# Kernel tuning notes

Hardware: AMD Instinct MI355X
Metric: run time of the kernel (lower is better)

## Reference

```python
import jax, jax.numpy as jnp
import numpy as np

EPS = 1e-6
NUM_HEADS = 4


def setup_inputs() -> dict:
    key = jax.random.key(0)
    ks = jax.random.split(key, 7)
    B, C, H, W = 4, 128, 64, 64
    x = jax.random.normal(ks[0], (B, C, H, W), dtype=jnp.float32)
    norm_w = jnp.ones((C,), dtype=jnp.float32)
    norm_b = jnp.zeros((C,), dtype=jnp.float32)
    # 1x1 convs stored as [out_ch, in_ch] matrices
    qkv_w = jax.random.normal(ks[1], (3 * C, C), dtype=jnp.float32) / np.sqrt(C)
    qkv_b = jnp.zeros((3 * C,), dtype=jnp.float32)
    proj_w = jax.random.normal(ks[2], (C, C), dtype=jnp.float32) / np.sqrt(C)
    proj_b = jnp.zeros((C,), dtype=jnp.float32)
    return {"x": x, "norm_w": norm_w, "norm_b": norm_b,
            "qkv_w": qkv_w, "qkv_b": qkv_b, "proj_w": proj_w, "proj_b": proj_b}


def reference(x, norm_w, norm_b, qkv_w, qkv_b, proj_w, proj_b):
    B, C, H, W = x.shape
    nh = NUM_HEADS
    dh = C // nh
    N = H * W

    # ChannelLayerNorm: stats over channel dim per spatial position
    mean = jnp.mean(x, axis=1, keepdims=True)
    var = jnp.mean(jnp.square(x - mean), axis=1, keepdims=True)  # unbiased=False
    h = (x - mean) * jax.lax.rsqrt(var + EPS)
    h = h * norm_w[None, :, None, None] + norm_b[None, :, None, None]

    # qkv 1x1 conv -> [B, 3C, H, W]
    qkv = jnp.einsum('oc,bchw->bohw', qkv_w, h) + qkv_b[None, :, None, None]
    qkv = qkv.reshape(B, 3, nh, dh, N)
    q, k, v = qkv[:, 0], qkv[:, 1], qkv[:, 2]  # each [B, nh, dh, N]

    scale = dh ** -0.5
    attn = jnp.einsum('bhcn,bhcm->bhnm', q, k) * scale  # [B, nh, N, N]
    attn = jax.nn.softmax(attn, axis=-1)
    h = jnp.einsum('bhnm,bhcm->bhcn', attn, v)  # [B, nh, dh, N]
    h = h.reshape(B, C, H, W)

    h = jnp.einsum('oc,bchw->bohw', proj_w, h) + proj_b[None, :, None, None]
    return x + h
```

## Files before the change

### kernel.cpp

```cpp
#include <hip/hip_runtime.h>
#include <hip/hip_bf16.h>
#include <math.h>

#define BB 4
#define CC 128
#define NH 4
#define DH 32
#define NN 4096
#define OC3 (3*CC)

typedef __attribute__((ext_vector_type(8))) short short8;
typedef __attribute__((ext_vector_type(4))) short short4v;
typedef __attribute__((ext_vector_type(4))) float float4v;

__device__ inline short f2bf(float f) {
    unsigned u = __builtin_bit_cast(unsigned, f);
    u += 0x7FFF + ((u >> 16) & 1);
    return (short)(u >> 16);
}
__device__ inline unsigned pk2bf(float a, float b) {
    __hip_bfloat162 h = __float22bfloat162_rn(make_float2(a, b));
    unsigned u; __builtin_memcpy(&u, &h, 4);
    return u;
}

#define HS 136
__global__ __launch_bounds__(512, 4) void lnqkv_kernel(
        const float* __restrict__ x, const float* __restrict__ nw,
        const float* __restrict__ nb, const float* __restrict__ qw,
        const float* __restrict__ qbias,
        short* __restrict__ qT, short* __restrict__ kT, short* __restrict__ vv) {
    __shared__ short hT[64 * HS];
    __shared__ float red[16][64];
    __shared__ float mrs[2][64];
    int t = threadIdx.x;
    int n0g = blockIdx.x * 64;
    int b = n0g >> 12, n0 = n0g & (NN - 1);
    int nl = t & 63, cq = t >> 6;

    const float* xp = x + ((size_t)b * CC + cq * 16) * NN + n0 + nl;
    float xv[16];
    float s = 0.f, ss = 0.f;
    #pragma unroll
    for (int j = 0; j < 16; ++j) {
        xv[j] = xp[(size_t)j * NN];
        s += xv[j]; ss += xv[j] * xv[j];
    }
    red[cq][nl] = s; red[cq + 8][nl] = ss;
    __syncthreads();
    if (t < 64) {
        float s8 = 0.f, q8 = 0.f;
        #pragma unroll
        for (int j = 0; j < 8; ++j) { s8 += red[j][t]; q8 += red[j + 8][t]; }
        float mean = s8 * (1.0f / CC);
        float var  = q8 * (1.0f / CC) - mean * mean;
        mrs[0][t] = mean;
        mrs[1][t] = rsqrtf(var + 1e-6f);
    }
    __syncthreads();
    {
        float mean = mrs[0][nl], rsv = mrs[1][nl];
        #pragma unroll
        for (int j = 0; j < 16; j += 8) {
            union { short8 v; unsigned u[4]; } z;
            #pragma unroll
            for (int k = 0; k < 4; ++k) {
                int c = cq * 16 + j + 2 * k;
                float h0 = (xv[j + 2 * k]     - mean) * rsv * nw[c]     + nb[c];
                float h1 = (xv[j + 2 * k + 1] - mean) * rsv * nw[c + 1] + nb[c + 1];
                z.u[k] = pk2bf(h0, h1);
            }
            *(short8*)&hT[nl * HS + cq * 16 + j] = z.v;
        }
    }
    __syncthreads();

    int w = t >> 6, lane = t & 63;
    int lg = lane >> 4, ln = lane & 15;
    #pragma unroll
    for (int it = 0; it < 3; ++it) {
        int ow = (w + it * 8) * 16;
        const float* wp = qw + (size_t)(ow + ln) * CC;
        float4v a0 = {0,0,0,0}, a1 = {0,0,0,0}, a2 = {0,0,0,0}, a3 = {0,0,0,0};
        #pragma unroll
        for (int cs = 0; cs < 4; ++cs) {
            float4 wa = *(const float4*)(wp + cs * 32 + lg * 8);
            float4 wb = *(const float4*)(wp + cs * 32 + lg * 8 + 4);
            union { short8 v; unsigned u[4]; } af;
            af.u[0] = pk2bf(wa.x, wa.y); af.u[1] = pk2bf(wa.z, wa.w);
            af.u[2] = pk2bf(wb.x, wb.y); af.u[3] = pk2bf(wb.z, wb.w);
            const short* hp = &hT[cs * 32 + lg * 8];
            a0 = __builtin_amdgcn_mfma_f32_16x16x32_bf16(af.v, *(const short8*)&hp[(0  + ln) * HS], a0, 0, 0, 0);
            a1 = __builtin_amdgcn_mfma_f32_16x16x32_bf16(af.v, *(const short8*)&hp[(16 + ln) * HS], a1, 0, 0, 0);
            a2 = __builtin_amdgcn_mfma_f32_16x16x32_bf16(af.v, *(const short8*)&hp[(32 + ln) * HS], a2, 0, 0, 0);
            a3 = __builtin_amdgcn_mfma_f32_16x16x32_bf16(af.v, *(const short8*)&hp[(48 + ln) * HS], a3, 0, 0, 0);
        }
        int r0 = ow + lg * 4;
        float b0 = qbias[r0], b1 = qbias[r0 + 1], b2 = qbias[r0 + 2], b3 = qbias[r0 + 3];
        int cb = ow & 31;
        float4v* accs[4] = {&a0, &a1, &a2, &a3};
        if (it == 0) {
            const float qs = 0.1767766952966369f * 1.4426950408889634f;
            int hh = ow >> 5;
            size_t rowbase = (size_t)(b * NH + hh) * NN + n0;
            #pragma unroll
            for (int nsub = 0; nsub < 4; ++nsub) {
                float4v av = *accs[nsub];
                union { short4v v; unsigned u[2]; } z;
                z.u[0] = pk2bf((av.x + b0) * qs, (av.y + b1) * qs);
                z.u[1] = pk2bf((av.z + b2) * qs, (av.w + b3) * qs);
                *(short4v*)&qT[(rowbase + nsub * 16 + ln) * DH + cb + lg * 4] = z.v;
            }
        } else if (it == 1) {
            int hh = (ow - CC) >> 5;
            size_t rowbase = (size_t)(b * NH + hh) * NN + n0;
            #pragma unroll
            for (int nsub = 0; nsub < 4; ++nsub) {
                float4v av = *accs[nsub];
                union { short4v v; unsigned u[2]; } z;
                z.u[0] = pk2bf(av.x + b0, av.y + b1);
                z.u[1] = pk2bf(av.z + b2, av.w + b3);
                *(short4v*)&kT[(rowbase + nsub * 16 + ln) * DH + cb + lg * 4] = z.v;
            }
        } else {
            int hh = (ow - 2 * CC) >> 5;
            size_t cbase = (size_t)((b * NH + hh) * DH + cb + lg * 4);
            #pragma unroll
            for (int nsub = 0; nsub < 4; ++nsub) {
                float4v av = *accs[nsub];
                size_t col = (size_t)n0 + nsub * 16 + ln;
                vv[(cbase + 0) * NN + col] = f2bf(av.x + b0);
                vv[(cbase + 1) * NN + col] = f2bf(av.y + b1);
                vv[(cbase + 2) * NN + col] = f2bf(av.z + b2);
                vv[(cbase + 3) * NN + col] = f2bf(av.w + b3);
            }
        }
    }
}

#define PS 72
union __align__(16) FlashSh {
    short pt[8 * 16 * PS];
    struct { float mo[3][8][64][8]; float ml[3][8][64]; } m;
};
__global__ __launch_bounds__(512, 2) void flash_kernel(
        const short* __restrict__ qT, const short* __restrict__ kT,
        const short* __restrict__ vv, short* __restrict__ aoT) {
    __shared__ FlashSh sh;
    int blk = blockIdx.x;
    int bh = blk >> 5;
    int qb = blk & 31;
    int b = bh >> 2, hh = bh & 3;
    int n0 = qb * 128;
    int t = threadIdx.x, w = t >> 6, lane = t & 63;
    int lg = lane >> 4, ln = lane & 15;
    int qg = w & 1;
    int split = w >> 1;

    const short* kbase = kT + (size_t)bh * NN * DH + lg * 8;
    const short* vb0 = vv + ((size_t)bh * DH + ln) * NN + lg * 8;
    const short* vb1 = vb0 + (size_t)16 * NN;

    short8 qf[4];
    #pragma unroll
    for (int j = 0; j < 4; ++j)
        qf[j] = *(const short8*)&qT[((size_t)bh * NN + n0 + (qg * 4 + j) * 16 + ln) * DH + lg * 8];

    float4v o0[4], o1[4];
    float ls[4];
    #pragma unroll
    for (int j = 0; j < 4; ++j) {
        o0[j] = (float4v){0,0,0,0}; o1[j] = (float4v){0,0,0,0}; ls[j] = 0.f;
    }
    short* ptw = &sh.pt[w * 16 * PS];

    int mbeg = split * (NN / 4), mend = mbeg + NN / 4;
    for (int m0 = mbeg; m0 < mend; m0 += 64) {
        const short* kp = kbase + (size_t)m0 * DH;
        short8 k0 = *(const short8*)(kp + (size_t)(ln +  0) * DH);
        short8 k1 = *(const short8*)(kp + (size_t)(ln + 16) * DH);
        short8 k2 = *(const short8*)(kp + (size_t)(ln + 32) * DH);
        short8 k3 = *(const short8*)(kp + (size_t)(ln + 48) * DH);
        short8 v0 = *(const short8*)(vb0 + m0);
        short8 v1 = *(const short8*)(vb0 + m0 + 32);
        short8 v2 = *(const short8*)(vb1 + m0);
        short8 v3 = *(const short8*)(vb1 + m0 + 32);

        #pragma unroll
        for (int j = 0; j < 4; ++j) {
            float4v s0 = {0,0,0,0}, s1 = s0, s2 = s0, s3 = s0;
            s0 = __builtin_amdgcn_mfma_f32_16x16x32_bf16(k0, qf[j], s0, 0, 0, 0);
            s1 = __builtin_amdgcn_mfma_f32_16x16x32_bf16(k1, qf[j], s1, 0, 0, 0);
            s2 = __builtin_amdgcn_mfma_f32_16x16x32_bf16(k2, qf[j], s2, 0, 0, 0);
            s3 = __builtin_amdgcn_mfma_f32_16x16x32_bf16(k3, qf[j], s3, 0, 0, 0);
            float lacc = 0.f;
            float4v* sv[4] = {&s0, &s1, &s2, &s3};
            #pragma unroll
            for (int jj = 0; jj < 4; ++jj) {
                float4v sj = *sv[jj];
                float p0 = __builtin_amdgcn_exp2f(sj.x);
                float p1 = __builtin_amdgcn_exp2f(sj.y);
                float p2 = __builtin_amdgcn_exp2f(sj.z);
                float p3 = __builtin_amdgcn_exp2f(sj.w);
                lacc += (p0 + p1) + (p2 + p3);
                union { short4v v; unsigned u[2]; } z;
                z.u[0] = pk2bf(p0, p1); z.u[1] = pk2bf(p2, p3);
                *(short4v*)&ptw[ln * PS + jj * 16 + lg * 4] = z.v;
            }
            ls[j] += lacc;
            short8 pb0 = *(const short8*)&ptw[ln * PS + 0  + lg * 8];
            short8 pb1 = *(const short8*)&ptw[ln * PS + 32 + lg * 8];
            o0[j] = __builtin_amdgcn_mfma_f32_16x16x32_bf16(v0, pb0, o0[j], 0, 0, 0);
            o1[j] = __builtin_amdgcn_mfma_f32_16x16x32_bf16(v2, pb0, o1[j], 0, 0, 0);
            o0[j] = __builtin_amdgcn_mfma_f32_16x16x32_bf16(v1, pb1, o0[j], 0, 0, 0);
            o1[j] = __builtin_amdgcn_mfma_f32_16x16x32_bf16(v3, pb1, o1[j], 0, 0, 0);
        }
    }

    __syncthreads();
    if (split > 0) {
        int si = split - 1;
        #pragma unroll
        for (int j = 0; j < 4; ++j) {
            int tid = qg * 4 + j;
            float* mp = &sh.m.mo[si][tid][lane][0];
            *(float4*)(mp + 0) = make_float4(o0[j].x, o0[j].y, o0[j].z, o0[j].w);
            *(float4*)(mp + 4) = make_float4(o1[j].x, o1[j].y, o1[j].z, o1[j].w);
            sh.m.ml[si][tid][lane] = ls[j];
        }
    }
    __syncthreads();
    if (split == 0) {
        #pragma unroll
        for (int j = 0; j < 4; ++j) {
            int tid = qg * 4 + j;
            #pragma unroll
            for (int si = 0; si < 3; ++si) {
                const float* mp = &sh.m.mo[si][tid][lane][0];
                float4 a0 = *(const float4*)(mp + 0);
                float4 a1 = *(const float4*)(mp + 4);
                o0[j].x += a0.x; o0[j].y += a0.y; o0[j].z += a0.z; o0[j].w += a0.w;
                o1[j].x += a1.x; o1[j].y += a1.y; o1[j].z += a1.z; o1[j].w += a1.w;
                ls[j] += sh.m.ml[si][tid][lane];
            }
            float lt = ls[j];
            lt += __shfl_xor(lt, 16, 64);
            lt += __shfl_xor(lt, 32, 64);
            float inv = 1.0f / lt;
            short* ap = aoT + ((size_t)b * NN + n0 + tid * 16 + ln) * CC + hh * DH;
            union { short4v v; unsigned u[2]; } z;
            z.u[0] = pk2bf(o0[j].x * inv, o0[j].y * inv);
            z.u[1] = pk2bf(o0[j].z * inv, o0[j].w * inv);
            *(short4v*)&ap[lg * 4] = z.v;
            z.u[0] = pk2bf(o1[j].x * inv, o1[j].y * inv);
            z.u[1] = pk2bf(o1[j].z * inv, o1[j].w * inv);
            *(short4v*)&ap[16 + lg * 4] = z.v;
        }
    }
}

__global__ __launch_bounds__(256) void proj_kernel(
        const short* __restrict__ aoT, const float* __restrict__ pw,
        const float* __restrict__ pb, const float* __restrict__ x,
        float* __restrict__ out) {
    int t = threadIdx.x;
    int n0g = blockIdx.x * 64;
    int b = n0g >> 12, n0 = n0g & (NN - 1);
    int o0 = blockIdx.y * 64;
    int wo = t >> 6, lane = t & 63;
    int lg = lane >> 4, ln = lane & 15;
    int ow = o0 + wo * 16;
    const float* wp = pw + (size_t)(ow + ln) * CC;
    const short* ap = aoT + (size_t)n0g * CC + lg * 8;
    float4v a0 = {0,0,0,0}, a1 = {0,0,0,0}, a2 = {0,0,0,0}, a3 = {0,0,0,0};
    #pragma unroll
    for (int cs = 0; cs < 4; ++cs) {
        float4 wa = *(const float4*)(wp + cs * 32 + lg * 8);
        float4 wb = *(const float4*)(wp + cs * 32 + lg * 8 + 4);
        union { short8 v; unsigned u[4]; } af;
        af.u[0] = pk2bf(wa.x, wa.y); af.u[1] = pk2bf(wa.z, wa.w);
        af.u[2] = pk2bf(wb.x, wb.y); af.u[3] = pk2bf(wb.z, wb.w);
        const short* hp = ap + cs * 32;
        a0 = __builtin_amdgcn_mfma_f32_16x16x32_bf16(af.v, *(const short8*)&hp[(size_t)(0  + ln) * CC], a0, 0, 0, 0);
        a1 = __builtin_amdgcn_mfma_f32_16x16x32_bf16(af.v, *(const short8*)&hp[(size_t)(16 + ln) * CC], a1, 0, 0, 0);
        a2 = __builtin_amdgcn_mfma_f32_16x16x32_bf16(af.v, *(const short8*)&hp[(size_t)(32 + ln) * CC], a2, 0, 0, 0);
        a3 = __builtin_amdgcn_mfma_f32_16x16x32_bf16(af.v, *(const short8*)&hp[(size_t)(48 + ln) * CC], a3, 0, 0, 0);
    }
    int r0 = ow + lg * 4;
    float b0 = pb[r0], b1 = pb[r0 + 1], b2 = pb[r0 + 2], b3 = pb[r0 + 3];
    const float* xbase = x   + ((size_t)b * CC + r0) * NN + n0 + ln;
    float*       obase = out + ((size_t)b * CC + r0) * NN + n0 + ln;
    float4v* accs[4] = {&a0, &a1, &a2, &a3};
    #pragma unroll
    for (int nsub = 0; nsub < 4; ++nsub) {
        float4v av = *accs[nsub];
        const float* xp = xbase + nsub * 16;
        float* op = obase + nsub * 16;
        op[(size_t)0 * NN] = av.x + b0 + xp[(size_t)0 * NN];
        op[(size_t)1 * NN] = av.y + b1 + xp[(size_t)1 * NN];
        op[(size_t)2 * NN] = av.z + b2 + xp[(size_t)2 * NN];
        op[(size_t)3 * NN] = av.w + b3 + xp[(size_t)3 * NN];
    }
}

extern "C" void kernel_launch(void* const* d_in, const int* in_sizes, int n_in,
                              void* d_out, int out_size, void* d_ws, size_t ws_size,
                              hipStream_t stream) {
    const float* x    = (const float*)d_in[0];
    const float* nw   = (const float*)d_in[1];
    const float* nb   = (const float*)d_in[2];
    const float* qkvw = (const float*)d_in[3];
    const float* qkvb = (const float*)d_in[4];
    const float* pw   = (const float*)d_in[5];
    const float* pb   = (const float*)d_in[6];
    float* out = (float*)d_out;

    short* qT  = (short*)d_ws;
    short* kT  = qT + (size_t)BB * NH * NN * DH;
    short* vv  = kT + (size_t)BB * NH * NN * DH;
    short* aoT = vv + (size_t)BB * NH * DH * NN;

    lnqkv_kernel<<<dim3(256), 512, 0, stream>>>(x, nw, nb, qkvw, qkvb, qT, kT, vv);
    flash_kernel<<<dim3(512), 512, 0, stream>>>(qT, kT, vv, aoT);
    proj_kernel<<<dim3(256, 2), 256, 0, stream>>>(aoT, pw, pb, x, out);
}
```

Baseline: 145.7 us.

## Shrink flash blocks to 32 queries with 4 KV-split waves and tree merge

Each flash block now covers 32 queries with 256 threads: 4 waves, each handling a quarter of the keys, instead of 128 queries with 8 waves. The grid grows from 512 to 2048 blocks, and the cross-wave reduction becomes a two-level tree in shared memory. The aim is more blocks per CU and better load balance across the GPU. The cost is that each wave handles 2 query tiles instead of 4, so K/V loads are reused across fewer queries and global K/V traffic per query rises about twofold.

```diff
diff --git a/kernel.cpp b/kernel.cpp
--- a/kernel.cpp
+++ b/kernel.cpp
@@ -140,36 +140,35 @@
 
 #define PS 72
 union __align__(16) FlashSh {
-    short pt[8 * 16 * PS];
-    struct { float mo[3][8][64][8]; float ml[3][8][64]; } m;
+    short pt[4 * 16 * PS];
+    struct { float mo[2][2][64][8]; float ml[2][2][64]; } m;
 };
-__global__ __launch_bounds__(512, 2) void flash_kernel(
+__global__ __launch_bounds__(256, 8) void flash_kernel(
         const short* __restrict__ qT, const short* __restrict__ kT,
         const short* __restrict__ vv, short* __restrict__ aoT) {
     __shared__ FlashSh sh;
     int blk = blockIdx.x;
-    int bh = blk >> 5;
-    int qb = blk & 31;
+    int bh = blk >> 7;
+    int qb = blk & 127;
     int b = bh >> 2, hh = bh & 3;
-    int n0 = qb * 128;
+    int n0 = qb * 32;
     int t = threadIdx.x, w = t >> 6, lane = t & 63;
     int lg = lane >> 4, ln = lane & 15;
-    int qg = w & 1;
-    int split = w >> 1;
+    int split = w;
 
     const short* kbase = kT + (size_t)bh * NN * DH + lg * 8;
     const short* vb0 = vv + ((size_t)bh * DH + ln) * NN + lg * 8;
     const short* vb1 = vb0 + (size_t)16 * NN;
 
-    short8 qf[4];
-    #pragma unroll
-    for (int j = 0; j < 4; ++j)
-        qf[j] = *(const short8*)&qT[((size_t)bh * NN + n0 + (qg * 4 + j) * 16 + ln) * DH + lg * 8];
-
-    float4v o0[4], o1[4];
-    float ls[4];
-    #pragma unroll
-    for (int j = 0; j < 4; ++j) {
+    short8 qf[2];
+    #pragma unroll
+    for (int j = 0; j < 2; ++j)
+        qf[j] = *(const short8*)&qT[((size_t)bh * NN + n0 + j * 16 + ln) * DH + lg * 8];
+
+    float4v o0[2], o1[2];
+    float ls[2];
+    #pragma unroll
+    for (int j = 0; j < 2; ++j) {
         o0[j] = (float4v){0,0,0,0}; o1[j] = (float4v){0,0,0,0}; ls[j] = 0.f;
     }
     short* ptw = &sh.pt[w * 16 * PS];
@@ -187,7 +186,7 @@
         short8 v3 = *(const short8*)(vb1 + m0 + 32);
 
         #pragma unroll
-        for (int j = 0; j < 4; ++j) {
+        for (int j = 0; j < 2; ++j) {
             float4v s0 = {0,0,0,0}, s1 = s0, s2 = s0, s3 = s0;
             s0 = __builtin_amdgcn_mfma_f32_16x16x32_bf16(k0, qf[j], s0, 0, 0, 0);
             s1 = __builtin_amdgcn_mfma_f32_16x16x32_bf16(k1, qf[j], s1, 0, 0, 0);
@@ -218,36 +217,55 @@
     }
 
     __syncthreads();
-    if (split > 0) {
-        int si = split - 1;
-        #pragma unroll
-        for (int j = 0; j < 4; ++j) {
-            int tid = qg * 4 + j;
-            float* mp = &sh.m.mo[si][tid][lane][0];
+    if (split & 1) {
+        int slot = split >> 1;
+        #pragma unroll
+        for (int j = 0; j < 2; ++j) {
+            float* mp = &sh.m.mo[slot][j][lane][0];
             *(float4*)(mp + 0) = make_float4(o0[j].x, o0[j].y, o0[j].z, o0[j].w);
             *(float4*)(mp + 4) = make_float4(o1[j].x, o1[j].y, o1[j].z, o1[j].w);
-            sh.m.ml[si][tid][lane] = ls[j];
+            sh.m.ml[slot][j][lane] = ls[j];
+        }
+    }
+    __syncthreads();
+    if (!(split & 1)) {
+        int slot = split >> 1;
+        #pragma unroll
+        for (int j = 0; j < 2; ++j) {
+            const float* mp = &sh.m.mo[slot][j][lane][0];
+            float4 a0 = *(const float4*)(mp + 0);
+            float4 a1 = *(const float4*)(mp + 4);
+            o0[j].x += a0.x; o0[j].y += a0.y; o0[j].z += a0.z; o0[j].w += a0.w;
+            o1[j].x += a1.x; o1[j].y += a1.y; o1[j].z += a1.z; o1[j].w += a1.w;
+            ls[j] += sh.m.ml[slot][j][lane];
+        }
+    }
+    __syncthreads();
+    if (split == 2) {
+        #pragma unroll
+        for (int j = 0; j < 2; ++j) {
+            float* mp = &sh.m.mo[0][j][lane][0];
+            *(float4*)(mp + 0) = make_float4(o0[j].x, o0[j].y, o0[j].z, o0[j].w);
+            *(float4*)(mp + 4) = make_float4(o1[j].x, o1[j].y, o1[j].z, o1[j].w);
+            sh.m.ml[0][j][lane] = ls[j];
         }
     }
     __syncthreads();
     if (split == 0) {
         #pragma unroll
-        for (int j = 0; j < 4; ++j) {
-            int tid = qg * 4 + j;
-            #pragma unroll
-            for (int si = 0; si < 3; ++si) {
-                const float* mp = &sh.m.mo[si][tid][lane][0];
-                float4 a0 = *(const float4*)(mp + 0);
-                float4 a1 = *(const float4*)(mp + 4);
-                o0[j].x += a0.x; o0[j].y += a0.y; o0[j].z += a0.z; o0[j].w += a0.w;
-                o1[j].x += a1.x; o1[j].y += a1.y; o1[j].z += a1.z; o1[j].w += a1.w;
-                ls[j] += sh.m.ml[si][tid][lane];
-            }
+        for (int j = 0; j < 2; ++j) {
+            const float* mp = &sh.m.mo[0][j][lane][0];
+            float4 a0 = *(const float4*)(mp + 0);
+            float4 a1 = *(const float4*)(mp + 4);
+            o0[j].x += a0.x; o0[j].y += a0.y; o0[j].z += a0.z; o0[j].w += a0.w;
+            o1[j].x += a1.x; o1[j].y += a1.y; o1[j].z += a1.z; o1[j].w += a1.w;
+            ls[j] += sh.m.ml[0][j][lane];
+
             float lt = ls[j];
             lt += __shfl_xor(lt, 16, 64);
             lt += __shfl_xor(lt, 32, 64);
             float inv = 1.0f / lt;
-            short* ap = aoT + ((size_t)b * NN + n0 + tid * 16 + ln) * CC + hh * DH;
+            short* ap = aoT + ((size_t)b * NN + n0 + j * 16 + ln) * CC + hh * DH;
             union { short4v v; unsigned u[2]; } z;
             z.u[0] = pk2bf(o0[j].x * inv, o0[j].y * inv);
             z.u[1] = pk2bf(o0[j].z * inv, o0[j].w * inv);
@@ -321,6 +339,6 @@
     short* aoT = vv + (size_t)BB * NH * DH * NN;
 
     lnqkv_kernel<<<dim3(256), 512, 0, stream>>>(x, nw, nb, qkvw, qkvb, qT, kT, vv);
-    flash_kernel<<<dim3(512), 512, 0, stream>>>(qT, kT, vv, aoT);
+    flash_kernel<<<dim3(2048), 256, 0, stream>>>(qT, kT, vv, aoT);
     proj_kernel<<<dim3(256, 2), 256, 0, stream>>>(aoT, pw, pb, x, out);
 }
```

Result: slower. 393.4 us (+170.0%).
